# Optimization experiments

Measured on AMD Instinct MI355X. Metric: run time of the kernel, lower is better.

The kernel has to match this reference:

```python
import jax, jax.numpy as jnp
import numpy as np

# RT-DETR multi-scale deformable attention reference (PPMSDeformableAttention forward, value_mask=None)
SPATIAL_SHAPES = ((80, 80), (40, 40), (20, 20))  # (H, W) per level; sum(H*W) = 8400 = Len_v
NUM_HEADS = 8
NUM_LEVELS = 3
NUM_POINTS = 4


def _gather_corner(v_l, ix, iy, H, W):
    # v_l: [bs, heads, H*W, hd]; ix/iy: [bs, heads, N] int32 pixel indices (possibly out of range)
    valid = (ix >= 0) & (ix < W) & (iy >= 0) & (iy < H)
    idx = jnp.clip(iy, 0, H - 1) * W + jnp.clip(ix, 0, W - 1)
    g = jnp.take_along_axis(v_l, idx[..., None], axis=2)  # [bs, heads, N, hd]
    return jnp.where(valid[..., None], g, jnp.zeros((), v_l.dtype))


def _bilinear_sample(v_l, px, py, H, W):
    # grid_sample(align_corners=False, padding_mode='zeros') semantics.
    # v_l: [bs, heads, H*W, hd]; px/py: [bs, heads, N] continuous pixel coords
    x0 = jnp.floor(px).astype(jnp.int32)
    y0 = jnp.floor(py).astype(jnp.int32)
    x1, y1 = x0 + 1, y0 + 1
    wx1 = px - x0.astype(px.dtype)
    wy1 = py - y0.astype(py.dtype)
    wx0, wy0 = 1.0 - wx1, 1.0 - wy1
    out = (_gather_corner(v_l, x0, y0, H, W) * (wx0 * wy0)[..., None]
           + _gather_corner(v_l, x1, y0, H, W) * (wx1 * wy0)[..., None]
           + _gather_corner(v_l, x0, y1, H, W) * (wx0 * wy1)[..., None]
           + _gather_corner(v_l, x1, y1, H, W) * (wx1 * wy1)[..., None])
    return out  # [bs, heads, N, hd]


def setup_inputs() -> dict:
    key = jax.random.key(0)
    ks = jax.random.split(key, 8)
    bs, Lq, C = 32, 300, 256
    Lv = sum(h * w for h, w in SPATIAL_SHAPES)
    tp = NUM_HEADS * NUM_LEVELS * NUM_POINTS  # 96
    s = 1.0 / np.sqrt(C)
    return {
        "query": jax.random.normal(ks[0], (bs, Lq, C), jnp.float32),
        "reference_points": jax.random.uniform(ks[1], (bs, Lq, NUM_LEVELS, 4), jnp.float32, 0.05, 0.95),
        "value": jax.random.normal(ks[2], (bs, Lv, C), jnp.float32),
        "Wv": jax.random.normal(ks[3], (C, C), jnp.float32) * s,
        "bv": jnp.zeros((C,), jnp.float32),
        "Woff": jax.random.normal(ks[4], (C, tp * 2), jnp.float32) * (s * 0.1),
        "boff": jax.random.normal(ks[5], (tp * 2,), jnp.float32) * 0.5,
        "Watt": jax.random.normal(ks[6], (C, tp), jnp.float32) * s,
        "batt": jnp.zeros((tp,), jnp.float32),
        "Wout": jax.random.normal(ks[7], (C, C), jnp.float32) * s,
        "bout": jnp.zeros((C,), jnp.float32),
    }


def reference(query, reference_points, value, Wv, bv, Woff, boff, Watt, batt, Wout, bout):
    bs, Lq, C = query.shape
    H_, L, P = NUM_HEADS, NUM_LEVELS, NUM_POINTS
    hd = C // H_
    Lv = value.shape[1]

    # value projection -> [bs, heads, Lv, hd]
    v = (value @ Wv + bv).reshape(bs, Lv, H_, hd).transpose(0, 2, 1, 3)

    # sampling offsets and attention weights from query
    off = (query @ Woff + boff).reshape(bs, Lq, H_, L, P, 2)
    attw = jax.nn.softmax((query @ Watt + batt).reshape(bs, Lq, H_, L * P), axis=-1)
    attw = attw.reshape(bs, Lq, H_, L, P)

    # reference_points last dim == 4: (cx, cy, w, h) normalized
    ref_xy = reference_points[:, :, None, :, None, :2]  # [bs,Lq,1,L,1,2]
    ref_wh = reference_points[:, :, None, :, None, 2:]
    loc = ref_xy + off / P * ref_wh * 0.5  # [bs,Lq,H,L,P,2], normalized [0,1]

    out = jnp.zeros((bs, Lq, H_, hd), query.dtype)
    start = 0
    for l, (H, W) in enumerate(SPATIAL_SHAPES):
        v_l = v[:, :, start:start + H * W]  # [bs, heads, H*W, hd]
        start += H * W
        # normalized -> pixel coords (align_corners=False): p = loc * size - 0.5
        locl = loc[:, :, :, l]  # [bs, Lq, heads, P, 2]
        px = locl[..., 0] * W - 0.5
        py = locl[..., 1] * H - 0.5
        # [bs, Lq, heads, P] -> [bs, heads, Lq*P]
        px = px.transpose(0, 2, 1, 3).reshape(bs, H_, Lq * P)
        py = py.transpose(0, 2, 1, 3).reshape(bs, H_, Lq * P)
        sampled = _bilinear_sample(v_l, px, py, H, W)  # [bs, heads, Lq*P, hd]
        sampled = sampled.reshape(bs, H_, Lq, P, hd)
        out = out + jnp.einsum('bhqpd,bqhp->bqhd', sampled, attw[:, :, :, l])

    out = out.reshape(bs, Lq, C)
    return out @ Wout + bout
```

## Files before the change

kernel.cpp:

```cpp
#include <hip/hip_runtime.h>
#include <hip/hip_bf16.h>

#define BS 32
#define LQ 300
#define CDIM 256
#define HEADS 8
#define HD 32
#define NLEVELS 3
#define NPOINTS 4
#define LV 8400
#define NOA 288

typedef __attribute__((ext_vector_type(4))) float f32x4;
typedef __attribute__((ext_vector_type(8))) short short8;
typedef __attribute__((ext_vector_type(8))) unsigned short u16x8;
typedef __attribute__((ext_vector_type(4))) unsigned short u16x4;

__device__ __forceinline__ unsigned short f2bf(float f) {
    __hip_bfloat16 h = __float2bfloat16(f);
    return __bfloat16_as_ushort(h);
}
__device__ __forceinline__ float bf2f(unsigned short u) {
    union { unsigned u; float f; } v; v.u = ((unsigned)u) << 16;
    return v.f;
}

__global__ void prep_weights_kernel(
    const float* __restrict__ Wv, const float* __restrict__ Wout,
    const float* __restrict__ Woff, const float* __restrict__ Watt,
    unsigned short* __restrict__ WvT, unsigned short* __restrict__ WoutT,
    unsigned short* __restrict__ WoaT)
{
    const int bid = blockIdx.x;
    const int k = threadIdx.x;
    if (bid < 256) {
        WvT[bid * 256 + k] = f2bf(Wv[k * 256 + bid]);
    } else if (bid < 512) {
        const int n = bid - 256;
        WoutT[n * 256 + k] = f2bf(Wout[k * 256 + n]);
    } else {
        const int n = bid - 512;
        const float w = (n < 192) ? Woff[k * 192 + n] : Watt[k * 96 + (n - 192)];
        WoaT[n * 256 + k] = f2bf(w);
    }
}

#define BM 128
#define BKP 64
#define PADP 72
#define EPAD 264
#define NTP (CDIM / BKP)

__global__ __launch_bounds__(512) void proj_value_mfma(
    const float* __restrict__ value, const unsigned short* __restrict__ WvT,
    const float* __restrict__ bv, unsigned short* __restrict__ vout)
{
    __shared__ alignas(16) unsigned short lds_raw[27648];
    unsigned short* lds_w = lds_raw;
    unsigned short* lds_x = lds_raw + 256 * PADP;
    unsigned short* lds_ep = lds_raw;

    const int tid = threadIdx.x;
    const int lane = tid & 63;
    const int wave = tid >> 6;
    const int wm = wave >> 2;
    const int wn = wave & 3;
    const int la = lane & 15;
    const int lg = lane >> 4;

    const int orig = blockIdx.x;
    const int xcd = orig & 7, lin = orig >> 3;
    const int bid = (xcd < 4 ? xcd * 263 : 4 * 263 + (xcd - 4) * 262) + lin;
    const long row0 = (long)bid * BM;

    const int wr = tid >> 1, wk = (tid & 1) * 32;
    const unsigned short* wptr = WvT + (size_t)wr * CDIM + wk;
    const int xr = tid >> 2, xk = (tid & 3) * 16;
    const float* xptr = value + (row0 + xr) * (long)CDIM + xk;

    u16x8 wrg[4];
    f32x4 xrg[4];

    auto load_tile = [&](int kb) {
        const u16x8* qw = (const u16x8*)(wptr + kb);
        wrg[0] = qw[0]; wrg[1] = qw[1]; wrg[2] = qw[2]; wrg[3] = qw[3];
        const float* p = xptr + kb;
        xrg[0] = *(const f32x4*)(p);
        xrg[1] = *(const f32x4*)(p + 4);
        xrg[2] = *(const f32x4*)(p + 8);
        xrg[3] = *(const f32x4*)(p + 12);
    };
    auto write_tile = [&]() {
        u16x8* ww = (u16x8*)&lds_w[wr * PADP + wk];
        ww[0] = wrg[0]; ww[1] = wrg[1]; ww[2] = wrg[2]; ww[3] = wrg[3];
        u16x8 t0, t1;
#pragma unroll
        for (int i = 0; i < 4; ++i) {
            t0[i]     = f2bf(xrg[0][i]);
            t0[i + 4] = f2bf(xrg[1][i]);
            t1[i]     = f2bf(xrg[2][i]);
            t1[i + 4] = f2bf(xrg[3][i]);
        }
        u16x8* wx = (u16x8*)&lds_x[xr * PADP + xk];
        wx[0] = t0; wx[1] = t1;
    };

    f32x4 acc[4][4] = {};

    load_tile(0);

#pragma unroll
    for (int t = 0; t < NTP; ++t) {
        __syncthreads();
        write_tile();
        __syncthreads();
        if (t + 1 < NTP) load_tile((t + 1) * BKP);

#pragma unroll
        for (int kk = 0; kk < 2; ++kk) {
            const unsigned short* pw = &lds_w[(wn * 64 + la) * PADP + kk * 32 + lg * 8];
            const unsigned short* px = &lds_x[(wm * 64 + la) * PADP + kk * 32 + lg * 8];
            short8 xf[4];
#pragma unroll
            for (int mf = 0; mf < 4; ++mf)
                xf[mf] = *(const short8*)(px + mf * 16 * PADP);
#pragma unroll
            for (int nf = 0; nf < 4; ++nf) {
                const short8 wf = *(const short8*)(pw + nf * 16 * PADP);
#pragma unroll
                for (int mf = 0; mf < 4; ++mf)
                    acc[nf][mf] = __builtin_amdgcn_mfma_f32_16x16x32_bf16(
                        wf, xf[mf], acc[nf][mf], 0, 0, 0);
            }
        }
    }

#pragma unroll
    for (int pass = 0; pass < 2; ++pass) {
        __syncthreads();
        if (wm == pass) {
#pragma unroll
            for (int nf = 0; nf < 4; ++nf) {
                const int nbl = wn * 64 + nf * 16 + lg * 4;
                const f32x4 bb = *(const f32x4*)&bv[nbl];
#pragma unroll
                for (int mf = 0; mf < 4; ++mf) {
                    const int mloc = mf * 16 + la;
                    u16x4 o;
#pragma unroll
                    for (int j = 0; j < 4; ++j) o[j] = f2bf(acc[nf][mf][j] + bb[j]);
                    *(u16x4*)&lds_ep[mloc * EPAD + nbl] = o;
                }
            }
        }
        __syncthreads();
        const int er = tid >> 3;
        const int ec = (tid & 7) * 32;
        const long gr = row0 + pass * 64 + er;
        const u16x8* src = (const u16x8*)&lds_ep[er * EPAD + ec];
        u16x8* dst = (u16x8*)&vout[gr * CDIM + ec];
#pragma unroll
        for (int i = 0; i < 4; ++i) dst[i] = src[i];
    }
}

#define BMQ 128
#define BKQ 32
#define APAD 40
#define BPAD 40

__global__ __launch_bounds__(256) void offatt_gemm_mfma(
    const float* __restrict__ query, const unsigned short* __restrict__ WoaT,
    const float* __restrict__ boff, const float* __restrict__ batt,
    float* __restrict__ offatt)
{
    __shared__ unsigned short lds_a[2][BMQ * APAD];
    __shared__ unsigned short lds_b[2][NOA * BPAD];

    const int tid = threadIdx.x;
    const int lane = tid & 63;
    const int wave = tid >> 6;
    const int wm = wave >> 1;
    const int wn = wave & 1;
    const long row0 = (long)blockIdx.x * BMQ;

    const int ar = tid >> 1;
    const int ak = (tid & 1) * 16;
    const float* aptr = query + (row0 + ar) * CDIM + ak;
    const unsigned short* bptr  = WoaT + (size_t)tid * CDIM;
    const unsigned short* bptr2 = WoaT + (size_t)(256 + tid) * CDIM;
    const bool extra = tid < 32;

    f32x4 arg[4];
    u16x8 brg[4], brg2[4];

    auto load_tile = [&](int kb) {
        const float* p = aptr + kb;
        arg[0] = *(const f32x4*)(p);
        arg[1] = *(const f32x4*)(p + 4);
        arg[2] = *(const f32x4*)(p + 8);
        arg[3] = *(const f32x4*)(p + 12);
        const u16x8* q = (const u16x8*)(bptr + kb);
        brg[0] = q[0]; brg[1] = q[1]; brg[2] = q[2]; brg[3] = q[3];
        if (extra) {
            const u16x8* q2 = (const u16x8*)(bptr2 + kb);
            brg2[0] = q2[0]; brg2[1] = q2[1]; brg2[2] = q2[2]; brg2[3] = q2[3];
        }
    };
    auto write_tile = [&](int buf) {
        u16x8 t0, t1;
#pragma unroll
        for (int i = 0; i < 4; ++i) {
            t0[i]     = f2bf(arg[0][i]);
            t0[i + 4] = f2bf(arg[1][i]);
            t1[i]     = f2bf(arg[2][i]);
            t1[i + 4] = f2bf(arg[3][i]);
        }
        u16x8* wa = (u16x8*)&lds_a[buf][ar * APAD + ak];
        wa[0] = t0; wa[1] = t1;
        u16x8* wb = (u16x8*)&lds_b[buf][tid * BPAD];
        wb[0] = brg[0]; wb[1] = brg[1]; wb[2] = brg[2]; wb[3] = brg[3];
        if (extra) {
            u16x8* wb2 = (u16x8*)&lds_b[buf][(256 + tid) * BPAD];
            wb2[0] = brg2[0]; wb2[1] = brg2[1]; wb2[2] = brg2[2]; wb2[3] = brg2[3];
        }
    };

    f32x4 acc[4][9] = {};
    const int la = lane & 15;
    const int lg = lane >> 4;

    load_tile(0);
    write_tile(0);
    __syncthreads();
    int cur = 0;

    for (int t = 0; t < CDIM / BKQ; ++t) {
        if (t + 1 < CDIM / BKQ) load_tile((t + 1) * BKQ);

        const unsigned short* pa = &lds_a[cur][(wm * 64 + la) * APAD + lg * 8];
        const unsigned short* pb = &lds_b[cur][(wn * 144 + la) * BPAD + lg * 8];
        short8 af[4];
#pragma unroll
        for (int mi = 0; mi < 4; ++mi)
            af[mi] = *(const short8*)(pa + mi * 16 * APAD);
#pragma unroll
        for (int ni = 0; ni < 9; ++ni) {
            const short8 bf = *(const short8*)(pb + ni * 16 * BPAD);
#pragma unroll
            for (int mi = 0; mi < 4; ++mi)
                acc[mi][ni] = __builtin_amdgcn_mfma_f32_16x16x32_bf16(af[mi], bf, acc[mi][ni], 0, 0, 0);
        }

        if (t + 1 < CDIM / BKQ) write_tile(cur ^ 1);
        __syncthreads();
        cur ^= 1;
    }

    float bias[9];
#pragma unroll
    for (int ni = 0; ni < 9; ++ni) {
        const int col = wn * 144 + ni * 16 + la;
        bias[ni] = (col < 192) ? boff[col] : batt[col - 192];
    }
#pragma unroll
    for (int mi = 0; mi < 4; ++mi) {
#pragma unroll
        for (int ni = 0; ni < 9; ++ni) {
            const int col = wn * 144 + ni * 16 + la;
#pragma unroll
            for (int j = 0; j < 4; ++j) {
                const long r = row0 + wm * 64 + mi * 16 + lg * 4 + j;
                offatt[r * NOA + col] = acc[mi][ni][j] + bias[ni];
            }
        }
    }
}

__global__ __launch_bounds__(256) void sample_kernel(
    const float* __restrict__ offatt, const float* __restrict__ refpts,
    const unsigned short* __restrict__ v, unsigned short* __restrict__ mid)
{
    __shared__ float oa_s[NOA];
    __shared__ float aw_s[96];
    __shared__ float px_s[96];
    __shared__ float py_s[96];

    const int tid = threadIdx.x;
    const int nb = blockIdx.x;
    const int x = nb & 7;
    const int rest = nb >> 3;
    const int g = rest / LQ;
    const int q = rest % LQ;
    const int b = g * 8 + x;
    const long bq = (long)b * LQ + q;

    oa_s[tid] = offatt[bq * NOA + tid];
    if (tid < 32) oa_s[256 + tid] = offatt[bq * NOA + 256 + tid];
    __syncthreads();

    if (tid < 8) {
        float m = -1e30f;
#pragma unroll
        for (int i = 0; i < 12; ++i) m = fmaxf(m, oa_s[192 + tid * 12 + i]);
        float e[12];
        float s = 0.f;
#pragma unroll
        for (int i = 0; i < 12; ++i) { e[i] = __expf(oa_s[192 + tid * 12 + i] - m); s += e[i]; }
        const float inv = 1.f / s;
#pragma unroll
        for (int i = 0; i < 12; ++i) aw_s[tid * 12 + i] = e[i] * inv;
    }
    if (tid >= 128 && tid < 224) {
        const int t = tid - 128;
        const int h = t / 12, idx = t % 12, lvl = idx >> 2, p = idx & 3;
        const float* rp = refpts + (bq * NLEVELS + lvl) * 4;
        const float rx = rp[0], ry = rp[1], rw = rp[2], rh = rp[3];
        const float ox = oa_s[((h * NLEVELS + lvl) * NPOINTS + p) * 2 + 0];
        const float oy = oa_s[((h * NLEVELS + lvl) * NPOINTS + p) * 2 + 1];
        const float lx = rx + ox * 0.125f * rw;
        const float ly = ry + oy * 0.125f * rh;
        const int Wl = 80 >> lvl;
        px_s[t] = lx * (float)Wl - 0.5f;
        py_s[t] = ly * (float)Wl - 0.5f;
    }
    __syncthreads();

    const int h = tid >> 5;
    const int pg = (tid >> 3) & 3;
    const int d4 = tid & 7;
    const unsigned short* vb = v + ((size_t)b * LV) * CDIM + h * HD + d4 * 4;

    float a0 = 0.f, a1 = 0.f, a2 = 0.f, a3 = 0.f;
#pragma unroll
    for (int j = 0; j < 3; ++j) {
        const int i = pg * 3 + j;
        const int lvl = i >> 2;
        const int idx = h * 12 + i;
        const float px = px_s[idx], py = py_s[idx], aw = aw_s[idx];
        const int Wl = 80 >> lvl;
        const int start = (lvl == 0) ? 0 : (lvl == 1) ? 6400 : 8000;

        const float fx = floorf(px), fy = floorf(py);
        const int x0 = (int)fx, y0 = (int)fy;
        const float wx1 = px - fx, wy1 = py - fy;
        const float wx0 = 1.f - wx1, wy0 = 1.f - wy1;
        const float w00 = wx0 * wy0 * aw, w10 = wx1 * wy0 * aw;
        const float w01 = wx0 * wy1 * aw, w11 = wx1 * wy1 * aw;
        const bool x0v = (unsigned)x0 < (unsigned)Wl;
        const bool x1v = (unsigned)(x0 + 1) < (unsigned)Wl;
        const bool y0v = (unsigned)y0 < (unsigned)Wl;
        const bool y1v = (unsigned)(y0 + 1) < (unsigned)Wl;

        const unsigned short* base = vb + (size_t)start * CDIM;
        if (y0v) {
            const unsigned short* r0p = base + (size_t)(y0 * Wl) * CDIM;
            if (x0v) {
                const u16x4 u = *(const u16x4*)(r0p + (size_t)x0 * CDIM);
                a0 = fmaf(w00, bf2f(u[0]), a0); a1 = fmaf(w00, bf2f(u[1]), a1);
                a2 = fmaf(w00, bf2f(u[2]), a2); a3 = fmaf(w00, bf2f(u[3]), a3);
            }
            if (x1v) {
                const u16x4 u = *(const u16x4*)(r0p + (size_t)(x0 + 1) * CDIM);
                a0 = fmaf(w10, bf2f(u[0]), a0); a1 = fmaf(w10, bf2f(u[1]), a1);
                a2 = fmaf(w10, bf2f(u[2]), a2); a3 = fmaf(w10, bf2f(u[3]), a3);
            }
        }
        if (y1v) {
            const unsigned short* r1p = base + (size_t)((y0 + 1) * Wl) * CDIM;
            if (x0v) {
                const u16x4 u = *(const u16x4*)(r1p + (size_t)x0 * CDIM);
                a0 = fmaf(w01, bf2f(u[0]), a0); a1 = fmaf(w01, bf2f(u[1]), a1);
                a2 = fmaf(w01, bf2f(u[2]), a2); a3 = fmaf(w01, bf2f(u[3]), a3);
            }
            if (x1v) {
                const u16x4 u = *(const u16x4*)(r1p + (size_t)(x0 + 1) * CDIM);
                a0 = fmaf(w11, bf2f(u[0]), a0); a1 = fmaf(w11, bf2f(u[1]), a1);
                a2 = fmaf(w11, bf2f(u[2]), a2); a3 = fmaf(w11, bf2f(u[3]), a3);
            }
        }
    }

    a0 += __shfl_xor(a0, 8);  a1 += __shfl_xor(a1, 8);
    a2 += __shfl_xor(a2, 8);  a3 += __shfl_xor(a3, 8);
    a0 += __shfl_xor(a0, 16); a1 += __shfl_xor(a1, 16);
    a2 += __shfl_xor(a2, 16); a3 += __shfl_xor(a3, 16);

    if (pg == 0) {
        u16x4 o;
        o[0] = f2bf(a0); o[1] = f2bf(a1); o[2] = f2bf(a2); o[3] = f2bf(a3);
        *(u16x4*)&mid[bq * CDIM + h * HD + d4 * 4] = o;
    }
}

__global__ __launch_bounds__(256) void out_gemm_mfma(
    const unsigned short* __restrict__ mid, const unsigned short* __restrict__ WoutT,
    const float* __restrict__ bout, float* __restrict__ out)
{
    __shared__ unsigned short lds_w[2][256 * APAD];
    __shared__ unsigned short lds_x[2][BMQ * BPAD];

    const int tid = threadIdx.x;
    const int lane = tid & 63;
    const int wave = tid >> 6;
    const int wn = wave & 1;
    const int wm = wave >> 1;
    const long row0 = (long)blockIdx.x * BMQ;

    const unsigned short* wptr = WoutT + (size_t)tid * CDIM;
    const int xr = tid >> 1;
    const int xk = (tid & 1) * 16;
    const unsigned short* xptr = mid + (row0 + xr) * CDIM + xk;

    u16x8 wrg[4];
    u16x8 xrg[2];

    auto load_tile = [&](int kb) {
        const u16x8* qw = (const u16x8*)(wptr + kb);
        wrg[0] = qw[0]; wrg[1] = qw[1]; wrg[2] = qw[2]; wrg[3] = qw[3];
        const u16x8* qx = (const u16x8*)(xptr + kb);
        xrg[0] = qx[0]; xrg[1] = qx[1];
    };
    auto write_tile = [&](int buf) {
        u16x8* ww = (u16x8*)&lds_w[buf][tid * APAD];
        ww[0] = wrg[0]; ww[1] = wrg[1]; ww[2] = wrg[2]; ww[3] = wrg[3];
        u16x8* wx = (u16x8*)&lds_x[buf][xr * BPAD + xk];
        wx[0] = xrg[0]; wx[1] = xrg[1];
    };

    f32x4 acc[8][4] = {};
    const int la = lane & 15;
    const int lg = lane >> 4;

    load_tile(0);
    write_tile(0);
    __syncthreads();
    int cur = 0;

    for (int t = 0; t < CDIM / BKQ; ++t) {
        if (t + 1 < CDIM / BKQ) load_tile((t + 1) * BKQ);

        const unsigned short* pw = &lds_w[cur][(wn * 128 + la) * APAD + lg * 8];
        const unsigned short* px = &lds_x[cur][(wm * 64 + la) * BPAD + lg * 8];
        short8 xf[4];
#pragma unroll
        for (int mf = 0; mf < 4; ++mf)
            xf[mf] = *(const short8*)(px + mf * 16 * BPAD);
#pragma unroll
        for (int nf = 0; nf < 8; ++nf) {
            const short8 wf = *(const short8*)(pw + nf * 16 * APAD);
#pragma unroll
            for (int mf = 0; mf < 4; ++mf)
                acc[nf][mf] = __builtin_amdgcn_mfma_f32_16x16x32_bf16(wf, xf[mf], acc[nf][mf], 0, 0, 0);
        }

        if (t + 1 < CDIM / BKQ) write_tile(cur ^ 1);
        __syncthreads();
        cur ^= 1;
    }

#pragma unroll
    for (int nf = 0; nf < 8; ++nf) {
        const int nbase = wn * 128 + nf * 16 + lg * 4;
        const f32x4 bb = *(const f32x4*)&bout[nbase];
#pragma unroll
        for (int mf = 0; mf < 4; ++mf) {
            const long m = row0 + wm * 64 + mf * 16 + la;
            f32x4 o;
#pragma unroll
            for (int j = 0; j < 4; ++j) o[j] = acc[nf][mf][j] + bb[j];
            *(f32x4*)&out[m * CDIM + nbase] = o;
        }
    }
}

extern "C" void kernel_launch(void* const* d_in, const int* in_sizes, int n_in,
                              void* d_out, int out_size, void* d_ws, size_t ws_size,
                              hipStream_t stream) {
    const float* query = (const float*)d_in[0];
    const float* refp  = (const float*)d_in[1];
    const float* value = (const float*)d_in[2];
    const float* Wv    = (const float*)d_in[3];
    const float* bv    = (const float*)d_in[4];
    const float* Woff  = (const float*)d_in[5];
    const float* boff  = (const float*)d_in[6];
    const float* Watt  = (const float*)d_in[7];
    const float* batt  = (const float*)d_in[8];
    const float* Wout  = (const float*)d_in[9];
    const float* bout  = (const float*)d_in[10];
    float* out = (float*)d_out;

    char* ws = (char*)d_ws;
    unsigned short* v = (unsigned short*)ws;
    size_t off = (size_t)BS * LV * CDIM * 2;
    float* offatt = (float*)(ws + off);
    off += (size_t)BS * LQ * NOA * 4;
    unsigned short* mid = (unsigned short*)(ws + off);
    off += (size_t)BS * LQ * CDIM * 2;
    unsigned short* WvT = (unsigned short*)(ws + off);
    off += 256 * 256 * 2;
    unsigned short* WoaT = (unsigned short*)(ws + off);
    off += NOA * 256 * 2;
    unsigned short* WoutT = (unsigned short*)(ws + off);

    prep_weights_kernel<<<800, 256, 0, stream>>>(Wv, Wout, Woff, Watt, WvT, WoutT, WoaT);
    proj_value_mfma<<<(BS * LV) / BM, 512, 0, stream>>>(value, WvT, bv, v);
    offatt_gemm_mfma<<<(BS * LQ) / BMQ, 256, 0, stream>>>(query, WoaT, boff, batt, offatt);
    sample_kernel<<<BS * LQ, 256, 0, stream>>>(offatt, refp, v, mid);
    out_gemm_mfma<<<(BS * LQ) / BMQ, 256, 0, stream>>>(mid, WoutT, bout, out);
}
```

Measured before the change: 205.0 us.

## Fuse offset/attention GEMM into value projection kernel as extra blocks

Merges the query offset/attention-weight GEMM into the value-projection kernel launch: the first 75 blocks compute the offatt GEMM with 512 threads, and the rest run the original value projection. This removes a separate launch and lets the small GEMM overlap with the large one instead of running serially. In exchange the shared-memory footprint grows to the larger of the two needs, which can reduce occupancy for the value projection. The block index offset also changes the XCD-aware mapping.

After: 211.9 us. +3.4%, slower.

```diff
diff --git a/kernel.cpp b/kernel.cpp
--- a/kernel.cpp
+++ b/kernel.cpp
@@ -50,25 +50,125 @@
 #define PADP 72
 #define EPAD 264
 #define NTP (CDIM / BKP)
-
-__global__ __launch_bounds__(512) void proj_value_mfma(
+#define APAD 40
+#define BPAD 40
+#define BKQ 32
+#define NOFF 75
+
+__global__ __launch_bounds__(512) void proj_offatt_fused(
     const float* __restrict__ value, const unsigned short* __restrict__ WvT,
-    const float* __restrict__ bv, unsigned short* __restrict__ vout)
+    const float* __restrict__ bv, unsigned short* __restrict__ vout,
+    const float* __restrict__ query, const unsigned short* __restrict__ WoaT,
+    const float* __restrict__ boff, const float* __restrict__ batt,
+    float* __restrict__ offatt)
 {
-    __shared__ alignas(16) unsigned short lds_raw[27648];
+    __shared__ alignas(16) char smem[66560];
+
+    const int tid = threadIdx.x;
+    const int lane = tid & 63;
+    const int wave = tid >> 6;
+    const int la = lane & 15;
+    const int lg = lane >> 4;
+
+    if (blockIdx.x < NOFF) {
+        unsigned short* lds_a = (unsigned short*)smem;
+        unsigned short* lds_b = lds_a + 2 * 128 * APAD;
+        const long row0 = (long)blockIdx.x * BM;
+
+        const int wm = wave >> 1;
+        const int wn = wave & 1;
+
+        const int ar = tid >> 2;
+        const int ak = (tid & 3) * 8;
+        const float* aptr = query + (row0 + ar) * CDIM + ak;
+        const unsigned short* bptr = WoaT + (size_t)tid * CDIM;
+        const bool bact = tid < NOA;
+
+        f32x4 arg[2];
+        u16x8 brg[4];
+
+        auto load_tile = [&](int kb) {
+            const float* p = aptr + kb;
+            arg[0] = *(const f32x4*)(p);
+            arg[1] = *(const f32x4*)(p + 4);
+            if (bact) {
+                const u16x8* q = (const u16x8*)(bptr + kb);
+                brg[0] = q[0]; brg[1] = q[1]; brg[2] = q[2]; brg[3] = q[3];
+            }
+        };
+        auto write_tile = [&](int buf) {
+            u16x8 t0;
+#pragma unroll
+            for (int i = 0; i < 4; ++i) {
+                t0[i]     = f2bf(arg[0][i]);
+                t0[i + 4] = f2bf(arg[1][i]);
+            }
+            *(u16x8*)&lds_a[buf * (128 * APAD) + ar * APAD + ak] = t0;
+            if (bact) {
+                u16x8* wb = (u16x8*)&lds_b[buf * (NOA * BPAD) + tid * BPAD];
+                wb[0] = brg[0]; wb[1] = brg[1]; wb[2] = brg[2]; wb[3] = brg[3];
+            }
+        };
+
+        f32x4 acc[2][9] = {};
+
+        load_tile(0);
+        write_tile(0);
+        __syncthreads();
+        int cur = 0;
+
+        for (int t = 0; t < CDIM / BKQ; ++t) {
+            if (t + 1 < CDIM / BKQ) load_tile((t + 1) * BKQ);
+
+            const unsigned short* pa = &lds_a[cur * (128 * APAD) + (wm * 32 + la) * APAD + lg * 8];
+            const unsigned short* pb = &lds_b[cur * (NOA * BPAD) + (wn * 144 + la) * BPAD + lg * 8];
+            short8 af[2];
+#pragma unroll
+            for (int mi = 0; mi < 2; ++mi)
+                af[mi] = *(const short8*)(pa + mi * 16 * APAD);
+#pragma unroll
+            for (int ni = 0; ni < 9; ++ni) {
+                const short8 bf = *(const short8*)(pb + ni * 16 * BPAD);
+#pragma unroll
+                for (int mi = 0; mi < 2; ++mi)
+                    acc[mi][ni] = __builtin_amdgcn_mfma_f32_16x16x32_bf16(af[mi], bf, acc[mi][ni], 0, 0, 0);
+            }
+
+            if (t + 1 < CDIM / BKQ) write_tile(cur ^ 1);
+            __syncthreads();
+            cur ^= 1;
+        }
+
+        float bias[9];
+#pragma unroll
+        for (int ni = 0; ni < 9; ++ni) {
+            const int col = wn * 144 + ni * 16 + la;
+            bias[ni] = (col < 192) ? boff[col] : batt[col - 192];
+        }
+#pragma unroll
+        for (int mi = 0; mi < 2; ++mi) {
+#pragma unroll
+            for (int ni = 0; ni < 9; ++ni) {
+                const int col = wn * 144 + ni * 16 + la;
+#pragma unroll
+                for (int j = 0; j < 4; ++j) {
+                    const long r = row0 + wm * 32 + mi * 16 + lg * 4 + j;
+                    offatt[r * NOA + col] = acc[mi][ni][j] + bias[ni];
+                }
+            }
+        }
+        return;
+    }
+
+    unsigned short* lds_raw = (unsigned short*)smem;
     unsigned short* lds_w = lds_raw;
     unsigned short* lds_x = lds_raw + 256 * PADP;
     unsigned short* lds_ep = lds_raw;
 
-    const int tid = threadIdx.x;
-    const int lane = tid & 63;
-    const int wave = tid >> 6;
     const int wm = wave >> 2;
     const int wn = wave & 3;
-    const int la = lane & 15;
-    const int lg = lane >> 4;
-
-    const int orig = blockIdx.x;
+
+    const int orig = blockIdx.x - NOFF;
     const int xcd = orig & 7, lin = orig >> 3;
     const int bid = (xcd < 4 ? xcd * 263 : 4 * 263 + (xcd - 4) * 262) + lin;
     const long row0 = (long)bid * BM;
@@ -164,119 +264,6 @@
     }
 }
 
-#define BMQ 128
-#define BKQ 32
-#define APAD 40
-#define BPAD 40
-
-__global__ __launch_bounds__(256) void offatt_gemm_mfma(
-    const float* __restrict__ query, const unsigned short* __restrict__ WoaT,
-    const float* __restrict__ boff, const float* __restrict__ batt,
-    float* __restrict__ offatt)
-{
-    __shared__ unsigned short lds_a[2][BMQ * APAD];
-    __shared__ unsigned short lds_b[2][NOA * BPAD];
-
-    const int tid = threadIdx.x;
-    const int lane = tid & 63;
-    const int wave = tid >> 6;
-    const int wm = wave >> 1;
-    const int wn = wave & 1;
-    const long row0 = (long)blockIdx.x * BMQ;
-
-    const int ar = tid >> 1;
-    const int ak = (tid & 1) * 16;
-    const float* aptr = query + (row0 + ar) * CDIM + ak;
-    const unsigned short* bptr  = WoaT + (size_t)tid * CDIM;
-    const unsigned short* bptr2 = WoaT + (size_t)(256 + tid) * CDIM;
-    const bool extra = tid < 32;
-
-    f32x4 arg[4];
-    u16x8 brg[4], brg2[4];
-
-    auto load_tile = [&](int kb) {
-        const float* p = aptr + kb;
-        arg[0] = *(const f32x4*)(p);
-        arg[1] = *(const f32x4*)(p + 4);
-        arg[2] = *(const f32x4*)(p + 8);
-        arg[3] = *(const f32x4*)(p + 12);
-        const u16x8* q = (const u16x8*)(bptr + kb);
-        brg[0] = q[0]; brg[1] = q[1]; brg[2] = q[2]; brg[3] = q[3];
-        if (extra) {
-            const u16x8* q2 = (const u16x8*)(bptr2 + kb);
-            brg2[0] = q2[0]; brg2[1] = q2[1]; brg2[2] = q2[2]; brg2[3] = q2[3];
-        }
-    };
-    auto write_tile = [&](int buf) {
-        u16x8 t0, t1;
-#pragma unroll
-        for (int i = 0; i < 4; ++i) {
-            t0[i]     = f2bf(arg[0][i]);
-            t0[i + 4] = f2bf(arg[1][i]);
-            t1[i]     = f2bf(arg[2][i]);
-            t1[i + 4] = f2bf(arg[3][i]);
-        }
-        u16x8* wa = (u16x8*)&lds_a[buf][ar * APAD + ak];
-        wa[0] = t0; wa[1] = t1;
-        u16x8* wb = (u16x8*)&lds_b[buf][tid * BPAD];
-        wb[0] = brg[0]; wb[1] = brg[1]; wb[2] = brg[2]; wb[3] = brg[3];
-        if (extra) {
-            u16x8* wb2 = (u16x8*)&lds_b[buf][(256 + tid) * BPAD];
-            wb2[0] = brg2[0]; wb2[1] = brg2[1]; wb2[2] = brg2[2]; wb2[3] = brg2[3];
-        }
-    };
-
-    f32x4 acc[4][9] = {};
-    const int la = lane & 15;
-    const int lg = lane >> 4;
-
-    load_tile(0);
-    write_tile(0);
-    __syncthreads();
-    int cur = 0;
-
-    for (int t = 0; t < CDIM / BKQ; ++t) {
-        if (t + 1 < CDIM / BKQ) load_tile((t + 1) * BKQ);
-
-        const unsigned short* pa = &lds_a[cur][(wm * 64 + la) * APAD + lg * 8];
-        const unsigned short* pb = &lds_b[cur][(wn * 144 + la) * BPAD + lg * 8];
-        short8 af[4];
-#pragma unroll
-        for (int mi = 0; mi < 4; ++mi)
-            af[mi] = *(const short8*)(pa + mi * 16 * APAD);
-#pragma unroll
-        for (int ni = 0; ni < 9; ++ni) {
-            const short8 bf = *(const short8*)(pb + ni * 16 * BPAD);
-#pragma unroll
-            for (int mi = 0; mi < 4; ++mi)
-                acc[mi][ni] = __builtin_amdgcn_mfma_f32_16x16x32_bf16(af[mi], bf, acc[mi][ni], 0, 0, 0);
-        }
-
-        if (t + 1 < CDIM / BKQ) write_tile(cur ^ 1);
-        __syncthreads();
-        cur ^= 1;
-    }
-
-    float bias[9];
-#pragma unroll
-    for (int ni = 0; ni < 9; ++ni) {
-        const int col = wn * 144 + ni * 16 + la;
-        bias[ni] = (col < 192) ? boff[col] : batt[col - 192];
-    }
-#pragma unroll
-    for (int mi = 0; mi < 4; ++mi) {
-#pragma unroll
-        for (int ni = 0; ni < 9; ++ni) {
-            const int col = wn * 144 + ni * 16 + la;
-#pragma unroll
-            for (int j = 0; j < 4; ++j) {
-                const long r = row0 + wm * 64 + mi * 16 + lg * 4 + j;
-                offatt[r * NOA + col] = acc[mi][ni][j] + bias[ni];
-            }
-        }
-    }
-}
-
 __global__ __launch_bounds__(256) void sample_kernel(
     const float* __restrict__ offatt, const float* __restrict__ refpts,
     const unsigned short* __restrict__ v, unsigned short* __restrict__ mid)
@@ -398,14 +385,14 @@
     const float* __restrict__ bout, float* __restrict__ out)
 {
     __shared__ unsigned short lds_w[2][256 * APAD];
-    __shared__ unsigned short lds_x[2][BMQ * BPAD];
+    __shared__ unsigned short lds_x[2][BM * BPAD];
 
     const int tid = threadIdx.x;
     const int lane = tid & 63;
     const int wave = tid >> 6;
     const int wn = wave & 1;
     const int wm = wave >> 1;
-    const long row0 = (long)blockIdx.x * BMQ;
+    const long row0 = (long)blockIdx.x * BM;
 
     const unsigned short* wptr = WoutT + (size_t)tid * CDIM;
     const int xr = tid >> 1;
@@ -504,8 +491,8 @@
     unsigned short* WoutT = (unsigned short*)(ws + off);
 
     prep_weights_kernel<<<800, 256, 0, stream>>>(Wv, Wout, Woff, Watt, WvT, WoutT, WoaT);
-    proj_value_mfma<<<(BS * LV) / BM, 512, 0, stream>>>(value, WvT, bv, v);
-    offatt_gemm_mfma<<<(BS * LQ) / BMQ, 256, 0, stream>>>(query, WoaT, boff, batt, offatt);
+    proj_offatt_fused<<<NOFF + (BS * LV) / BM, 512, 0, stream>>>(
+        value, WvT, bv, v, query, WoaT, boff, batt, offatt);
     sample_kernel<<<BS * LQ, 256, 0, stream>>>(offatt, refp, v, mid);
-    out_gemm_mfma<<<(BS * LQ) / BMQ, 256, 0, stream>>>(mid, WoutT, bout, out);
-}
+    out_gemm_mfma<<<(BS * LQ) / BM, 256, 0, stream>>>(mid, WoutT, bout, out);
+}
```
